# Kernel optimization log

Measured on AMD Instinct MI355X. Metric: run time of the kernel, lower is better.

The kernel has to match this reference:

```python
import jax, jax.numpy as jnp
import numpy as np

SEQ = 4096
D_EMB = 2048
D_HEAD = 128
SCALE = 0.02


def setup_inputs() -> dict:
    key = jax.random.key(0)
    kx, kq, kk, kv, ko = jax.random.split(key, 5)
    x = jax.random.normal(kx, (SEQ, D_EMB), dtype=jnp.float32)
    W_Q = jax.random.normal(kq, (D_EMB, D_EMB), dtype=jnp.float32) * SCALE
    W_K = jax.random.normal(kk, (D_EMB, D_EMB), dtype=jnp.float32) * SCALE
    W_V = jax.random.normal(kv, (D_EMB, D_EMB), dtype=jnp.float32) * SCALE
    W_O = jax.random.normal(ko, (D_EMB, D_EMB), dtype=jnp.float32) * SCALE
    b_Q = jnp.zeros((D_EMB,), dtype=jnp.float32)
    b_K = jnp.zeros((D_EMB,), dtype=jnp.float32)
    b_V = jnp.zeros((D_EMB,), dtype=jnp.float32)
    b_O = jnp.zeros((D_EMB,), dtype=jnp.float32)
    return {"x": x, "W_Q": W_Q, "W_K": W_K, "W_V": W_V, "W_O": W_O,
            "b_Q": b_Q, "b_K": b_K, "b_V": b_V, "b_O": b_O, "d_head": D_HEAD}


def reference(x, W_Q, W_K, W_V, W_O, b_Q, b_K, b_V, b_O, d_head):
    # x: [S, D]
    q = x @ W_Q + b_Q  # [S, D]
    k = x @ W_K + b_K
    v = x @ W_V + b_V
    scores = (q @ k.T) / jnp.sqrt(jnp.float32(d_head))  # [S, S]
    seq = scores.shape[0]
    causal = jnp.tril(jnp.ones((seq, seq), dtype=bool))
    scores = jnp.where(causal, scores, -jnp.inf)
    weights = jax.nn.softmax(scores, axis=-1)  # [S, S]
    attn_out = weights @ v  # [S, D]
    return attn_out @ W_O + b_O
```

## Files before the change

### kernel.cpp

```cpp
#include <hip/hip_runtime.h>
#include <hip/hip_fp16.h>

typedef _Float16 f16;
typedef _Float16 f16x8 __attribute__((ext_vector_type(8)));
typedef _Float16 f16x4 __attribute__((ext_vector_type(4)));
typedef float    f32x4 __attribute__((ext_vector_type(4)));

#define SEQ      4096
#define DEMB     2048
#define SCALE_QK 0.08838834764831845f

#define GAS __attribute__((address_space(1)))
#define LAS __attribute__((address_space(3)))

__device__ __forceinline__ void load_lds16(const f16* g, f16* l) {
    __builtin_amdgcn_global_load_lds((const GAS void*)g, (LAS void*)l, 16, 0, 0);
}

__device__ __forceinline__ f16x8 ldsr(const f16* base, int byteoff) {
    byteoff ^= (byteoff >> 3) & 0x70;
    return *(const f16x8*)((const char*)base + byteoff);
}

__device__ __forceinline__ void stage_half(const f16* __restrict__ src, int ldk,
                                           f16* ldsdst, int tid) {
#pragma unroll
    for (int s = 0; s < 2; ++s) {
        const int o   = s * 8192 + tid * 16;
        const int osw = o ^ ((o >> 3) & 0x70);
        load_lds16(src + (size_t)(osw >> 7) * ldk + ((osw & 127) >> 1),
                   ldsdst + (s * 8192 + (tid >> 6) * 1024) / 2);
    }
}

template <int MODE>
__device__ __forceinline__ void gemm_core(
        const f16* __restrict__ A, int lda, const f16* __restrict__ BT, int ldb,
        void* __restrict__ outp, int ldo, const float* __restrict__ bias,
        int bm, int bn, int NI, int kt0, float scale, f16* lds) {
    const int m0 = bm * 256, n0 = bn * 256;

    const int tid  = threadIdx.x;
    const int lane = tid & 63;
    const int wr   = (tid >> 6) >> 2;
    const int wc   = (tid >> 6) & 3;
    const int fr   = lane & 15;
    const int kb   = (lane >> 4) * 16;

    const f16* Abase = A + (size_t)m0 * lda + kt0 * 64;
    const f16* Bbase = BT + (size_t)n0 * ldb + kt0 * 64;

#define STG(buf, isB, half, t) \
    stage_half((isB) ? (Bbase + (size_t)((half) * 128) * ldb + (t) * 64) \
                     : (Abase + (size_t)((half) * 128) * lda + (t) * 64), \
               (isB) ? ldb : lda, \
               lds + (buf) * 32768 + (isB) * 16384 + (half) * 8192, tid)

    f32x4 acc[8][4] = {};
    f16x8 af[8], bf0[4], bf1[4];

#define READ_A(Mh, buf) { \
    const f16* bb = lds + (buf) * 32768; \
    _Pragma("unroll") for (int m = 0; m < 4; ++m) \
    _Pragma("unroll") for (int ks = 0; ks < 2; ++ks) \
        af[m * 2 + ks] = ldsr(bb, ((Mh) * 128 + wr * 64 + m * 16 + fr) * 128 + ks * 64 + kb); }

#define READ_B(Nh, buf, dst) { \
    const f16* bb = lds + (buf) * 32768 + 16384; \
    _Pragma("unroll") for (int n = 0; n < 2; ++n) \
    _Pragma("unroll") for (int ks = 0; ks < 2; ++ks) \
        dst[n * 2 + ks] = ldsr(bb, ((Nh) * 128 + wc * 32 + n * 16 + fr) * 128 + ks * 64 + kb); }

#define MFMA_PH(Mh, Nh, bfx) { \
    __builtin_amdgcn_s_setprio(1); \
    _Pragma("unroll") for (int m = 0; m < 4; ++m) \
    _Pragma("unroll") for (int n = 0; n < 2; ++n) \
    _Pragma("unroll") for (int ks = 0; ks < 2; ++ks) \
        acc[(Mh) * 4 + m][(Nh) * 2 + n] = __builtin_amdgcn_mfma_f32_16x16x32_f16( \
            af[m * 2 + ks], bfx[n * 2 + ks], acc[(Mh) * 4 + m][(Nh) * 2 + n], 0, 0, 0); \
    __builtin_amdgcn_s_setprio(0); }

#define BAR   asm volatile("s_barrier" ::: "memory")
#define VM6   asm volatile("s_waitcnt vmcnt(6)" ::: "memory")
#define VM0   asm volatile("s_waitcnt vmcnt(0)" ::: "memory")

    STG(0, 0, 0, 0); STG(0, 1, 0, 0); STG(0, 1, 1, 0); STG(0, 0, 1, 0);
    STG(1, 0, 0, 1); STG(1, 1, 0, 1); STG(1, 1, 1, 1);
    VM6; BAR;

    for (int i = 0; i < NI; ++i) {
        const int t0 = 2 * i;
        const bool more = (i + 1 < NI);
        READ_A(0, 0); READ_B(0, 0, bf0);
        STG(1, 0, 1, t0 + 1);
        BAR; MFMA_PH(0, 0, bf0); BAR;
        READ_B(1, 0, bf1);
        if (more) STG(0, 0, 0, t0 + 2);
        BAR; MFMA_PH(0, 1, bf1); BAR;
        READ_A(1, 0);
        if (more) STG(0, 1, 0, t0 + 2);
        BAR; MFMA_PH(1, 0, bf0); BAR;
        if (more) { STG(0, 1, 1, t0 + 2); VM6; } else { VM0; }
        BAR; MFMA_PH(1, 1, bf1); BAR;
        READ_A(0, 1); READ_B(0, 1, bf0);
        if (more) STG(0, 0, 1, t0 + 2);
        BAR; MFMA_PH(0, 0, bf0); BAR;
        READ_B(1, 1, bf1);
        if (more) STG(1, 0, 0, t0 + 3);
        BAR; MFMA_PH(0, 1, bf1); BAR;
        READ_A(1, 1);
        if (more) STG(1, 1, 0, t0 + 3);
        BAR; MFMA_PH(1, 0, bf0); BAR;
        if (more) STG(1, 1, 1, t0 + 3);
        VM6;
        BAR; MFMA_PH(1, 1, bf1); BAR;
    }

    const int rq = (lane >> 4) * 4;
#pragma unroll
    for (int mi = 0; mi < 8; ++mi) {
        const int row = m0 + (mi >> 2) * 128 + wr * 64 + (mi & 3) * 16 + rq;
#pragma unroll
        for (int ni = 0; ni < 4; ++ni) {
            const int col = n0 + (ni >> 1) * 128 + wc * 32 + (ni & 1) * 16 + fr;
            if (MODE == 0) {
                f16* o = (f16*)outp;
                const float bv = bias[col];
#pragma unroll
                for (int r = 0; r < 4; ++r)
                    o[(size_t)(row + r) * ldo + col] = (f16)(acc[mi][ni][r] + bv);
            } else if (MODE == 1) {
                f16* o = (f16*)outp;
                f16x4 v;
#pragma unroll
                for (int r = 0; r < 4; ++r) v[r] = (f16)acc[mi][ni][r];
                *(f16x4*)&o[(size_t)col * ldo + row] = v;
            } else if (MODE == 2) {
                float* o = (float*)outp;
                const float bv = bias ? bias[col] : 0.f;
#pragma unroll
                for (int r = 0; r < 4; ++r)
                    atomicAdd(&o[(size_t)(row + r) * ldo + col], acc[mi][ni][r] + bv);
            } else {
                f16* o = (f16*)outp;
#pragma unroll
                for (int r = 0; r < 4; ++r)
                    o[(size_t)(row + r) * ldo + col] = (f16)(acc[mi][ni][r] * scale);
            }
        }
    }
#undef STG
#undef READ_A
#undef READ_B
#undef MFMA_PH
#undef BAR
#undef VM6
#undef VM0
}

__global__ __launch_bounds__(256) void cvt_f16(const float* __restrict__ in,
                                               f16* __restrict__ out, int n) {
    int i = (blockIdx.x * 256 + threadIdx.x) * 4;
    if (i >= n) return;
    float4 v = *(const float4*)&in[i];
    f16x4 o; o[0] = (f16)v.x; o[1] = (f16)v.y; o[2] = (f16)v.z; o[3] = (f16)v.w;
    *(f16x4*)&out[i] = o;
}

__global__ __launch_bounds__(256) void transpose_cvt3(
        const float* __restrict__ WQ, const float* __restrict__ WK,
        const float* __restrict__ WO,
        f16* __restrict__ wqkt, f16* __restrict__ wot) {
    __shared__ f16 tile[64][72];
    const int z = blockIdx.z;
    const float* in = z == 0 ? WQ : z == 1 ? WK : WO;
    f16* out = z == 0 ? wqkt : z == 1 ? wqkt + (size_t)DEMB * DEMB : wot;
    const int c0 = blockIdx.x * 64, r0 = blockIdx.y * 64;
    const int tx = threadIdx.x & 63, ty = threadIdx.x >> 6;
    for (int rr = ty; rr < 64; rr += 4)
        tile[tx][rr] = (f16)in[(size_t)(r0 + rr) * DEMB + c0 + tx];
    __syncthreads();
    for (int cc = ty; cc < 64; cc += 4)
        out[(size_t)(c0 + cc) * DEMB + r0 + tx] = tile[cc][tx];
}

__global__ __launch_bounds__(512, 2)
void k_qk(const f16* __restrict__ x16, const f16* __restrict__ wqkt,
          f16* __restrict__ qk16, const float* __restrict__ bqk) {
    __shared__ f16 lds[65536];
    gemm_core<0>(x16, DEMB, wqkt, DEMB, qk16, 2 * DEMB, bqk,
                 blockIdx.y, blockIdx.x, 16, 0, 1.f, lds);
}

__global__ __launch_bounds__(512, 2)
void k_scores_wvo(const f16* __restrict__ qk16, f16* __restrict__ sb,
                  const f16* __restrict__ wv16, const f16* __restrict__ wot,
                  f16* __restrict__ wvoT) {
    __shared__ f16 lds[65536];
    const int bid = blockIdx.x;
    if (bid < 136) {
        int bm = (int)((sqrtf(8.f * bid + 1.f) - 1.f) * 0.5f);
        while ((bm + 1) * (bm + 2) / 2 <= bid) ++bm;
        while (bm * (bm + 1) / 2 > bid) --bm;
        const int bn = bid - bm * (bm + 1) / 2;
        gemm_core<3>(qk16, 2 * DEMB, qk16 + DEMB, 2 * DEMB, sb, SEQ, nullptr,
                     bm, bn, 16, 0, SCALE_QK, lds);
    } else {
        const int w = bid - 136;
        gemm_core<1>(wv16, DEMB, wot, DEMB, wvoT, DEMB, nullptr,
                     w >> 3, w & 7, 16, 0, 1.f, lds);
    }
}

__global__ __launch_bounds__(256) void k_softmax(f16* __restrict__ sb) {
    __shared__ f16 srow[SEQ];
    __shared__ float red[8];
    const int i  = blockIdx.x;
    const int L  = i + 1;
    const int Lp = ((i >> 8) + 1) << 8;
    f16* row = sb + (size_t)i * SEQ;
    const int t = threadIdx.x;

    float mx = -3.0e38f;
    for (int j0 = t * 8; j0 < Lp; j0 += 2048) {
        f16x8 v = *(const f16x8*)&row[j0];
        *(f16x8*)&srow[j0] = v;
#pragma unroll
        for (int u = 0; u < 8; ++u)
            if (j0 + u < L) mx = fmaxf(mx, (float)v[u]);
    }
#pragma unroll
    for (int o = 32; o > 0; o >>= 1) mx = fmaxf(mx, __shfl_xor(mx, o));
    if ((t & 63) == 0) red[t >> 6] = mx;
    __syncthreads();
    mx = fmaxf(fmaxf(red[0], red[1]), fmaxf(red[2], red[3]));

    float sm = 0.f;
    for (int j0 = t * 8; j0 < Lp; j0 += 2048) {
        f16x8 v = *(const f16x8*)&srow[j0];
#pragma unroll
        for (int u = 0; u < 8; ++u)
            if (j0 + u < L) sm += __expf((float)v[u] - mx);
    }
#pragma unroll
    for (int o = 32; o > 0; o >>= 1) sm += __shfl_xor(sm, o);
    if ((t & 63) == 0) red[4 + (t >> 6)] = sm;
    __syncthreads();
    const float inv = 1.f / (red[4] + red[5] + red[6] + red[7]);

    for (int j0 = t * 8; j0 < Lp; j0 += 2048) {
        f16x8 v = *(const f16x8*)&srow[j0];
        f16x8 wv;
#pragma unroll
        for (int u = 0; u < 8; ++u)
            wv[u] = (j0 + u < L) ? (f16)(__expf((float)v[u] - mx) * inv) : (f16)0.f;
        *(f16x8*)&row[j0] = wv;
    }
}

__global__ __launch_bounds__(512, 2)
void k_vw_bias(const f16* __restrict__ x16, const f16* __restrict__ wvoT,
               f16* __restrict__ vwT, const float* __restrict__ WO,
               const float* __restrict__ bV, float* __restrict__ bc) {
    __shared__ f16 lds[65536];
    const int bid = blockIdx.x;
    if (bid < 128) {
        gemm_core<1>(x16, DEMB, wvoT, DEMB, vwT, SEQ, nullptr,
                     bid >> 3, bid & 7, 16, 0, 1.f, lds);
        return;
    }
    const int b  = bid - 128;
    const int j0 = (b & 7) * 256;
    const int i0 = (b >> 3) * 256 + (threadIdx.x >> 8) * 128;
    const int jj = threadIdx.x & 255;
    float acc = 0.f;
    for (int i = i0; i < i0 + 128; ++i)
        acc += bV[i] * WO[(size_t)i * DEMB + j0 + jj];
    atomicAdd(&bc[j0 + jj], acc);
}

__global__ __launch_bounds__(512, 2)
void k_pvw(const f16* __restrict__ sb, const f16* __restrict__ vwT,
           float* __restrict__ out, const float* __restrict__ bc) {
    __shared__ f16 lds[65536];
    static const short BMt[30] = {0,1,2,3,4,5,6,6,7,7,8,8,9,9,10,10,11,11,
                                  12,12,12,13,13,13,14,14,14,15,15,15};
    static const short KT0t[30] = {0,0,0,0,0,0,0,14,0,16,0,18,0,20,0,22,0,24,
                                   0,18,36,0,20,38,0,20,40,0,22,44};
    static const short NIt[30] = {2,4,6,8,10,12,7,7,8,8,9,9,10,10,11,11,12,12,
                                  9,9,8,10,9,9,10,10,10,11,11,10};
    const int e = blockIdx.x, bn = blockIdx.y;
    const int bm = BMt[e], kt0 = KT0t[e], ni = NIt[e];
    gemm_core<2>(sb, SEQ, vwT, SEQ, out, DEMB, kt0 == 0 ? bc : nullptr,
                 bm, bn, ni, kt0, 1.f, lds);
}

extern "C" void kernel_launch(void* const* d_in, const int* in_sizes, int n_in,
                              void* d_out, int out_size, void* d_ws, size_t ws_size,
                              hipStream_t stream) {
    const float* x  = (const float*)d_in[0];
    const float* WQ = (const float*)d_in[1];
    const float* WK = (const float*)d_in[2];
    const float* WV = (const float*)d_in[3];
    const float* WO = (const float*)d_in[4];
    const float* bQ = (const float*)d_in[5];
    const float* bK = (const float*)d_in[6];
    const float* bV = (const float*)d_in[7];
    const float* bO = (const float*)d_in[8];
    float* out = (float*)d_out;

    char* w = (char*)d_ws;
    f16* qk16 = (f16*)w; w += (size_t)SEQ * 2 * DEMB * 2;
    f16* sb   = (f16*)w; w += (size_t)SEQ * SEQ * 2;
    f16* x16  = (f16*)w; w += (size_t)SEQ * DEMB * 2;
    f16* wqkt = (f16*)w; w += (size_t)2 * DEMB * DEMB * 2;
    f16* wv16 = (f16*)w; w += (size_t)DEMB * DEMB * 2;
    f16* wot  = (f16*)w; w += (size_t)DEMB * DEMB * 2;
    f16* wvoT = (f16*)w; w += (size_t)DEMB * DEMB * 2;
    float* bqk = (float*)w; w += 2 * DEMB * 4;
    float* bc  = (float*)w; w += DEMB * 4 + 4096;
    f16* vwT = wqkt;

    cvt_f16<<<(SEQ * DEMB) / 1024, 256, 0, stream>>>(x, x16, SEQ * DEMB);
    cvt_f16<<<(DEMB * DEMB) / 1024, 256, 0, stream>>>(WV, wv16, DEMB * DEMB);
    transpose_cvt3<<<dim3(DEMB / 64, DEMB / 64, 3), 256, 0, stream>>>(
        WQ, WK, WO, wqkt, wot);
    hipMemcpyAsync(bqk, bQ, DEMB * 4, hipMemcpyDeviceToDevice, stream);
    hipMemcpyAsync(bqk + DEMB, bK, DEMB * 4, hipMemcpyDeviceToDevice, stream);
    hipMemcpyAsync(bc, bO, DEMB * 4, hipMemcpyDeviceToDevice, stream);

    k_qk<<<dim3(2 * DEMB / 256, SEQ / 256), 512, 0, stream>>>(
        x16, wqkt, qk16, bqk);

    k_scores_wvo<<<200, 512, 0, stream>>>(qk16, sb, wv16, wot, wvoT);

    k_softmax<<<SEQ, 256, 0, stream>>>(sb);

    k_vw_bias<<<192, 512, 0, stream>>>(x16, wvoT, vwT, WO, bV, bc);

    hipMemsetAsync(out, 0, (size_t)SEQ * DEMB * 4, stream);
    k_pvw<<<dim3(30, 8), 512, 0, stream>>>(sb, vwT, out, bc);
}
```

Before: 323.4 us.

## Rebalance GEMM work across launches and store non-split output rows directly

Regroups the launches so the QK projection is split into two 128-block halves. The first half is co-scheduled with the W_V·W_O product and the bias reduction, and the second half with the x·(W_V W_O) product. Scores then run as their own 136-tile kernel. This balances each grid at 256 blocks and removes the separate vw_bias launch. The first six PV row blocks, which are not K-split, now use plain stores instead of atomics, so the output memset only covers the remaining rows. The vwT buffer moves to the wv16 slot so it no longer aliases the QK weights still needed in the second mixed kernel.

```diff
diff --git a/kernel.cpp b/kernel.cpp
--- a/kernel.cpp
+++ b/kernel.cpp
@@ -37,7 +37,7 @@
 __device__ __forceinline__ void gemm_core(
         const f16* __restrict__ A, int lda, const f16* __restrict__ BT, int ldb,
         void* __restrict__ outp, int ldo, const float* __restrict__ bias,
-        int bm, int bn, int NI, int kt0, float scale, f16* lds) {
+        int bm, int bn, int NI, int kt0, float scale, f16* lds, bool excl) {
     const int m0 = bm * 256, n0 = bn * 256;
 
     const int tid  = threadIdx.x;
@@ -138,9 +138,15 @@
             } else if (MODE == 2) {
                 float* o = (float*)outp;
                 const float bv = bias ? bias[col] : 0.f;
-#pragma unroll
-                for (int r = 0; r < 4; ++r)
-                    atomicAdd(&o[(size_t)(row + r) * ldo + col], acc[mi][ni][r] + bv);
+                if (excl) {
+#pragma unroll
+                    for (int r = 0; r < 4; ++r)
+                        o[(size_t)(row + r) * ldo + col] = acc[mi][ni][r] + bv;
+                } else {
+#pragma unroll
+                    for (int r = 0; r < 4; ++r)
+                        atomicAdd(&o[(size_t)(row + r) * ldo + col], acc[mi][ni][r] + bv);
+                }
             } else {
                 f16* o = (f16*)outp;
 #pragma unroll
@@ -185,31 +191,58 @@
 }
 
 __global__ __launch_bounds__(512, 2)
-void k_qk(const f16* __restrict__ x16, const f16* __restrict__ wqkt,
-          f16* __restrict__ qk16, const float* __restrict__ bqk) {
-    __shared__ f16 lds[65536];
-    gemm_core<0>(x16, DEMB, wqkt, DEMB, qk16, 2 * DEMB, bqk,
-                 blockIdx.y, blockIdx.x, 16, 0, 1.f, lds);
-}
-
-__global__ __launch_bounds__(512, 2)
-void k_scores_wvo(const f16* __restrict__ qk16, f16* __restrict__ sb,
-                  const f16* __restrict__ wv16, const f16* __restrict__ wot,
-                  f16* __restrict__ wvoT) {
+void k_mix1(const f16* __restrict__ x16, const f16* __restrict__ wqkt,
+            f16* __restrict__ qk16, const float* __restrict__ bqk,
+            const f16* __restrict__ wv16, const f16* __restrict__ wot,
+            f16* __restrict__ wvoT, const float* __restrict__ WO,
+            const float* __restrict__ bV, float* __restrict__ bc) {
     __shared__ f16 lds[65536];
     const int bid = blockIdx.x;
-    if (bid < 136) {
-        int bm = (int)((sqrtf(8.f * bid + 1.f) - 1.f) * 0.5f);
-        while ((bm + 1) * (bm + 2) / 2 <= bid) ++bm;
-        while (bm * (bm + 1) / 2 > bid) --bm;
-        const int bn = bid - bm * (bm + 1) / 2;
-        gemm_core<3>(qk16, 2 * DEMB, qk16 + DEMB, 2 * DEMB, sb, SEQ, nullptr,
-                     bm, bn, 16, 0, SCALE_QK, lds);
+    if (bid < 128) {
+        gemm_core<0>(x16, DEMB, wqkt, DEMB, qk16, 2 * DEMB, bqk,
+                     bid >> 4, bid & 15, 16, 0, 1.f, lds, false);
+    } else if (bid < 192) {
+        const int w = bid - 128;
+        gemm_core<1>(wv16, DEMB, wot, DEMB, wvoT, DEMB, nullptr,
+                     w >> 3, w & 7, 16, 0, 1.f, lds, false);
     } else {
-        const int w = bid - 136;
-        gemm_core<1>(wv16, DEMB, wot, DEMB, wvoT, DEMB, nullptr,
-                     w >> 3, w & 7, 16, 0, 1.f, lds);
-    }
+        const int b  = bid - 192;
+        const int j0 = (b & 7) * 256;
+        const int i0 = (b >> 3) * 256 + (threadIdx.x >> 8) * 128;
+        const int jj = threadIdx.x & 255;
+        float acc = 0.f;
+        for (int i = i0; i < i0 + 128; ++i)
+            acc += bV[i] * WO[(size_t)i * DEMB + j0 + jj];
+        atomicAdd(&bc[j0 + jj], acc);
+    }
+}
+
+__global__ __launch_bounds__(512, 2)
+void k_mix2(const f16* __restrict__ x16, const f16* __restrict__ wqkt,
+            f16* __restrict__ qk16, const float* __restrict__ bqk,
+            const f16* __restrict__ wvoT, f16* __restrict__ vwT) {
+    __shared__ f16 lds[65536];
+    const int bid = blockIdx.x;
+    if (bid < 128) {
+        gemm_core<0>(x16, DEMB, wqkt, DEMB, qk16, 2 * DEMB, bqk,
+                     8 + (bid >> 4), bid & 15, 16, 0, 1.f, lds, false);
+    } else {
+        const int b = bid - 128;
+        gemm_core<1>(x16, DEMB, wvoT, DEMB, vwT, SEQ, nullptr,
+                     b >> 3, b & 7, 16, 0, 1.f, lds, false);
+    }
+}
+
+__global__ __launch_bounds__(512, 2)
+void k_scores(const f16* __restrict__ qk16, f16* __restrict__ sb) {
+    __shared__ f16 lds[65536];
+    const int bid = blockIdx.x;
+    int bm = (int)((sqrtf(8.f * bid + 1.f) - 1.f) * 0.5f);
+    while ((bm + 1) * (bm + 2) / 2 <= bid) ++bm;
+    while (bm * (bm + 1) / 2 > bid) --bm;
+    const int bn = bid - bm * (bm + 1) / 2;
+    gemm_core<3>(qk16, 2 * DEMB, qk16 + DEMB, 2 * DEMB, sb, SEQ, nullptr,
+                 bm, bn, 16, 0, SCALE_QK, lds, false);
 }
 
 __global__ __launch_bounds__(256) void k_softmax(f16* __restrict__ sb) {
@@ -256,27 +289,6 @@
             wv[u] = (j0 + u < L) ? (f16)(__expf((float)v[u] - mx) * inv) : (f16)0.f;
         *(f16x8*)&row[j0] = wv;
     }
-}
-
-__global__ __launch_bounds__(512, 2)
-void k_vw_bias(const f16* __restrict__ x16, const f16* __restrict__ wvoT,
-               f16* __restrict__ vwT, const float* __restrict__ WO,
-               const float* __restrict__ bV, float* __restrict__ bc) {
-    __shared__ f16 lds[65536];
-    const int bid = blockIdx.x;
-    if (bid < 128) {
-        gemm_core<1>(x16, DEMB, wvoT, DEMB, vwT, SEQ, nullptr,
-                     bid >> 3, bid & 7, 16, 0, 1.f, lds);
-        return;
-    }
-    const int b  = bid - 128;
-    const int j0 = (b & 7) * 256;
-    const int i0 = (b >> 3) * 256 + (threadIdx.x >> 8) * 128;
-    const int jj = threadIdx.x & 255;
-    float acc = 0.f;
-    for (int i = i0; i < i0 + 128; ++i)
-        acc += bV[i] * WO[(size_t)i * DEMB + j0 + jj];
-    atomicAdd(&bc[j0 + jj], acc);
 }
 
 __global__ __launch_bounds__(512, 2)
@@ -292,7 +304,7 @@
     const int e = blockIdx.x, bn = blockIdx.y;
     const int bm = BMt[e], kt0 = KT0t[e], ni = NIt[e];
     gemm_core<2>(sb, SEQ, vwT, SEQ, out, DEMB, kt0 == 0 ? bc : nullptr,
-                 bm, bn, ni, kt0, 1.f, lds);
+                 bm, bn, ni, kt0, 1.f, lds, e < 6);
 }
 
 extern "C" void kernel_launch(void* const* d_in, const int* in_sizes, int n_in,
@@ -319,7 +331,7 @@
     f16* wvoT = (f16*)w; w += (size_t)DEMB * DEMB * 2;
     float* bqk = (float*)w; w += 2 * DEMB * 4;
     float* bc  = (float*)w; w += DEMB * 4 + 4096;
-    f16* vwT = wqkt;
+    f16* vwT = wv16;
 
     cvt_f16<<<(SEQ * DEMB) / 1024, 256, 0, stream>>>(x, x16, SEQ * DEMB);
     cvt_f16<<<(DEMB * DEMB) / 1024, 256, 0, stream>>>(WV, wv16, DEMB * DEMB);
@@ -329,15 +341,16 @@
     hipMemcpyAsync(bqk + DEMB, bK, DEMB * 4, hipMemcpyDeviceToDevice, stream);
     hipMemcpyAsync(bc, bO, DEMB * 4, hipMemcpyDeviceToDevice, stream);
 
-    k_qk<<<dim3(2 * DEMB / 256, SEQ / 256), 512, 0, stream>>>(
-        x16, wqkt, qk16, bqk);
-
-    k_scores_wvo<<<200, 512, 0, stream>>>(qk16, sb, wv16, wot, wvoT);
+    k_mix1<<<256, 512, 0, stream>>>(x16, wqkt, qk16, bqk, wv16, wot, wvoT,
+                                    WO, bV, bc);
+
+    k_mix2<<<256, 512, 0, stream>>>(x16, wqkt, qk16, bqk, wvoT, vwT);
+
+    k_scores<<<136, 512, 0, stream>>>(qk16, sb);
 
     k_softmax<<<SEQ, 256, 0, stream>>>(sb);
 
-    k_vw_bias<<<192, 512, 0, stream>>>(x16, wvoT, vwT, WO, bV, bc);
-
-    hipMemsetAsync(out, 0, (size_t)SEQ * DEMB * 4, stream);
+    hipMemsetAsync(out + (size_t)1536 * DEMB, 0,
+                   (size_t)(SEQ - 1536) * DEMB * 4, stream);
     k_pvw<<<dim3(30, 8), 512, 0, stream>>>(sb, vwT, out, bc);
 }
```

Measured after the change: 308.1 us. -4.7%, faster.
